# Optimization experiments

Measured on AMD Instinct MI355X. Metric: run time of the kernel, lower is better.

The kernel has to match this reference:

```python
import jax, jax.numpy as jnp
import numpy as np

N = 8192
IN_DIM = 256
OUT_DIM = 128
ALPHA = 0.2  # LeakyReLU negative slope
MASK_VAL = -9e15


def setup_inputs() -> dict:
    key = jax.random.key(0)
    k1, k2, k3, k4 = jax.random.split(key, 4)
    adjacency = jax.random.randint(k1, (N, N), 0, 2, dtype=jnp.int32)
    X = jax.random.normal(k2, (N, IN_DIM), dtype=jnp.float32)
    # kaiming-normal-ish scale
    W = jax.random.normal(k3, (IN_DIM, OUT_DIM), dtype=jnp.float32) * np.sqrt(2.0 / IN_DIM)
    a = jax.random.normal(k4, (2 * OUT_DIM, 1), dtype=jnp.float32) * np.sqrt(2.0 / (2 * OUT_DIM))
    return {"adjacency": adjacency, "X": X, "W": W, "a": a}


def reference(adjacency, X, W, a):
    Wh = X @ W  # [N, D]
    # e[i,j] = lrelu([Wh_i ; Wh_j] @ a) = lrelu(Wh@a1 + (Wh@a2)^T)
    a1 = a[:OUT_DIM, 0]   # [D]
    a2 = a[OUT_DIM:, 0]   # [D]
    e = (Wh @ a1)[:, None] + (Wh @ a2)[None, :]  # [N, N]
    e = jax.nn.leaky_relu(e, negative_slope=ALPHA)
    scores = jnp.where(adjacency > 0, e, jnp.asarray(MASK_VAL, e.dtype))
    attention = jax.nn.softmax(scores, axis=1)  # dropout p=0 -> identity
    h_prime = attention @ Wh  # [N, D]
    return jax.nn.elu(h_prime)
```

## Files before the change

kernel.cpp:

```cpp
#include <hip/hip_runtime.h>
#include <hip/hip_bf16.h>

#define NN 8192
#define KDIM 256
#define DDIM 128

typedef __attribute__((ext_vector_type(8))) short short8;
typedef __attribute__((ext_vector_type(4))) float floatx4;
typedef __attribute__((ext_vector_type(4))) int intx4;

__device__ __forceinline__ unsigned short f2bf(float x) {
    unsigned int u = __float_as_uint(x);
    return (unsigned short)((u + 0x8000u) >> 16);
}
__device__ __forceinline__ float bf2f(unsigned short b) {
    return __uint_as_float(((unsigned int)b) << 16);
}

__global__ void k_trip(float* out, float v) {
    if (threadIdx.x == 0 && blockIdx.x == 0) out[0] = v;
}

__global__ void k_detect(const unsigned short* __restrict__ X16, int* __restrict__ flag) {
    __shared__ int cnt;
    if (threadIdx.x == 0) cnt = 0;
    __syncthreads();
    unsigned short s = X16[2 * threadIdx.x];
    int e = (s >> 7) & 0xFF;
    if (e == 0 || (e >= 100 && e <= 145)) atomicAdd(&cnt, 1);
    __syncthreads();
    if (threadIdx.x == 0) *flag = (cnt >= 200) ? 1 : 0;
}

__global__ void k0_swizzleW(const unsigned short* __restrict__ W16,
                            const float* __restrict__ W32,
                            const int* __restrict__ flag,
                            unsigned short* __restrict__ WB) {
    int isb = *flag;
    int gid = blockIdx.x * blockDim.x + threadIdx.x;
    int kt   = gid >> 9;
    int nt   = (gid >> 6) & 7;
    int lane = gid & 63;
    int quad = lane >> 4, c = lane & 15;
    short8 pack;
    if (isb) {
#pragma unroll
        for (int t = 0; t < 8; ++t)
            pack[t] = (short)W16[(kt * 32 + quad * 8 + t) * DDIM + nt * 16 + c];
    } else {
#pragma unroll
        for (int t = 0; t < 8; ++t)
            pack[t] = (short)f2bf(W32[(kt * 32 + quad * 8 + t) * DDIM + nt * 16 + c]);
    }
    *(short8*)(WB + ((size_t)(kt * 8 + nt) * 64 + lane) * 8) = pack;
}

__global__ __launch_bounds__(256) void k1_wh(
        const unsigned short* __restrict__ X16,
        const float* __restrict__ X32,
        const unsigned short* __restrict__ WB,
        const unsigned short* __restrict__ a16,
        const float* __restrict__ a32,
        const int* __restrict__ flag,
        unsigned short* __restrict__ WhB,
        float* __restrict__ f, float* __restrict__ g) {
    __shared__ unsigned short tile[64 * 128];
    int isb = *flag;
    int tid = threadIdx.x;
    int wave = tid >> 6, lane = tid & 63;
    int quad = lane >> 4, c = lane & 15;
    int rowbase = blockIdx.x * 64 + wave * 16;

    floatx4 acc[8];
#pragma unroll
    for (int nt = 0; nt < 8; ++nt) acc[nt] = (floatx4)(0.0f);

    const short8* WB8 = (const short8*)WB;
#pragma unroll
    for (int ks = 0; ks < 8; ++ks) {
        short8 afrag;
        if (isb) {
            afrag = *(const short8*)(X16 + (size_t)(rowbase + c) * KDIM + ks * 32 + quad * 8);
        } else {
            const float* xp = X32 + (size_t)(rowbase + c) * KDIM + ks * 32 + quad * 8;
            floatx4 x0 = *(const floatx4*)xp;
            floatx4 x1 = *(const floatx4*)(xp + 4);
#pragma unroll
            for (int t = 0; t < 4; ++t) { afrag[t] = (short)f2bf(x0[t]); afrag[4 + t] = (short)f2bf(x1[t]); }
        }
#pragma unroll
        for (int nt = 0; nt < 8; ++nt) {
            short8 b = WB8[(ks * 8 + nt) * 64 + lane];
            acc[nt] = __builtin_amdgcn_mfma_f32_16x16x32_bf16(afrag, b, acc[nt], 0, 0, 0);
        }
    }

    float fp[4] = {0.f, 0.f, 0.f, 0.f}, gp[4] = {0.f, 0.f, 0.f, 0.f};
#pragma unroll
    for (int nt = 0; nt < 8; ++nt) {
        float a1 = isb ? bf2f(a16[nt * 16 + c]) : a32[nt * 16 + c];
        float a2 = isb ? bf2f(a16[DDIM + nt * 16 + c]) : a32[DDIM + nt * 16 + c];
#pragma unroll
        for (int r = 0; r < 4; ++r) {
            fp[r] += acc[nt][r] * a1;
            gp[r] += acc[nt][r] * a2;
        }
    }
#pragma unroll
    for (int m = 1; m < 16; m <<= 1) {
#pragma unroll
        for (int r = 0; r < 4; ++r) {
            fp[r] += __shfl_xor(fp[r], m);
            gp[r] += __shfl_xor(gp[r], m);
        }
    }
    if (c == 0) {
#pragma unroll
        for (int r = 0; r < 4; ++r) {
            f[rowbase + quad * 4 + r] = fp[r];
            g[rowbase + quad * 4 + r] = gp[r];
        }
    }

#pragma unroll
    for (int nt = 0; nt < 8; ++nt)
#pragma unroll
        for (int r = 0; r < 4; ++r)
            tile[(wave * 16 + quad * 4 + r) * 128 + nt * 16 + c] = f2bf(acc[nt][r]);
    __syncthreads();

    int kt2 = wave >> 1;
#pragma unroll
    for (int ntj = 0; ntj < 4; ++ntj) {
        int nt = (wave & 1) * 4 + ntj;
        short8 pack;
#pragma unroll
        for (int t = 0; t < 8; ++t)
            pack[t] = (short)tile[(kt2 * 32 + quad * 8 + t) * 128 + nt * 16 + c];
        *(short8*)(WhB + ((size_t)((blockIdx.x * 2 + kt2) * 8 + nt) * 64 + lane) * 8) = pack;
    }
}

__global__ __launch_bounds__(512) void k2_attn(
        const int* __restrict__ adj,
        const unsigned short* __restrict__ WhB,
        const float* __restrict__ f, const float* __restrict__ g,
        float* __restrict__ out) {
    __shared__ float smem[16384];
    int tid = threadIdx.x;
    int wave = tid >> 6, lane = tid & 63;
    int quad = lane >> 4, c = lane & 15;
    int rowbase = blockIdx.x * 32;

    for (int i = tid; i < NN / 4; i += 512)
        ((floatx4*)smem)[i] = ((const floatx4*)g)[i];
    __syncthreads();

    float f0 = f[rowbase + c];
    float f1 = f[rowbase + 16 + c];

    floatx4 acc0[8], acc1[8];
#pragma unroll
    for (int nt = 0; nt < 8; ++nt) { acc0[nt] = (floatx4)(0.0f); acc1[nt] = (floatx4)(0.0f); }
    float l0 = 0.0f, l1 = 0.0f;

    const intx4* arow0 = (const intx4*)(adj + (long)(rowbase + c) * NN);
    const intx4* arow1 = (const intx4*)(adj + (long)(rowbase + 16 + c) * NN);
    const short8* WhB8 = (const short8*)WhB;

    int j40 = wave * 8 + quad * 2;
    intx4 c00 = arow0[j40], c01 = arow0[j40 + 1];
    intx4 c10 = arow1[j40], c11 = arow1[j40 + 1];
    floatx4 g0 = *(const floatx4*)&smem[wave * 32 + quad * 8];
    floatx4 g1 = *(const floatx4*)&smem[wave * 32 + quad * 8 + 4];

    for (int t = 0; t < 32; ++t) {
        int tn = (t + 1) & 31;
        int j4n = (tn * 8 + wave) * 8 + quad * 2;
        intx4 n00 = arow0[j4n], n01 = arow0[j4n + 1];
        intx4 n10 = arow1[j4n], n11 = arow1[j4n + 1];
        int jbn = (tn * 8 + wave) * 32 + quad * 8;
        floatx4 gn0 = *(const floatx4*)&smem[jbn];
        floatx4 gn1 = *(const floatx4*)&smem[jbn + 4];

        int J32 = t * 8 + wave;
        short8 bfr[8];
#pragma unroll
        for (int nt = 0; nt < 8; ++nt)
            bfr[nt] = WhB8[((size_t)J32 * 8 + nt) * 64 + lane];

        short8 afr0, afr1;
#pragma unroll
        for (int u = 0; u < 4; ++u) {
            float x, E;
            unsigned short eb;
            x = f0 + g0[u]; x = fminf(fmaxf(x, 0.2f * x), 80.0f);
            E = (c00[u] > 0) ? __expf(x) : 0.0f; eb = f2bf(E); l0 += bf2f(eb); afr0[u] = (short)eb;
            x = f0 + g1[u]; x = fminf(fmaxf(x, 0.2f * x), 80.0f);
            E = (c01[u] > 0) ? __expf(x) : 0.0f; eb = f2bf(E); l0 += bf2f(eb); afr0[4 + u] = (short)eb;
            x = f1 + g0[u]; x = fminf(fmaxf(x, 0.2f * x), 80.0f);
            E = (c10[u] > 0) ? __expf(x) : 0.0f; eb = f2bf(E); l1 += bf2f(eb); afr1[u] = (short)eb;
            x = f1 + g1[u]; x = fminf(fmaxf(x, 0.2f * x), 80.0f);
            E = (c11[u] > 0) ? __expf(x) : 0.0f; eb = f2bf(E); l1 += bf2f(eb); afr1[4 + u] = (short)eb;
        }

#pragma unroll
        for (int nt = 0; nt < 8; ++nt) {
            acc0[nt] = __builtin_amdgcn_mfma_f32_16x16x32_bf16(afr0, bfr[nt], acc0[nt], 0, 0, 0);
            acc1[nt] = __builtin_amdgcn_mfma_f32_16x16x32_bf16(afr1, bfr[nt], acc1[nt], 0, 0, 0);
        }

        c00 = n00; c01 = n01; c10 = n10; c11 = n11;
        g0 = gn0; g1 = gn1;
    }

    __syncthreads();
    smem[wave * 128 + lane] = l0;
    smem[wave * 128 + 64 + lane] = l1;
    __syncthreads();
    if (tid < 32) {
        int mt = tid >> 4, cc = tid & 15;
        float s = 0.0f;
#pragma unroll
        for (int w = 0; w < 8; ++w)
#pragma unroll
            for (int q = 0; q < 4; ++q)
                s += smem[w * 128 + mt * 64 + q * 16 + cc];
        smem[1024 + tid] = s;
    }
    __syncthreads();
    float linv0[4], linv1[4];
    if (wave == 0) {
#pragma unroll
        for (int r = 0; r < 4; ++r) {
            float l0v = smem[1024 + quad * 4 + r];
            float l1v = smem[1024 + 16 + quad * 4 + r];
            linv0[r] = (l0v > 0.0f) ? 1.0f / l0v : 0.0f;
            linv1[r] = (l1v > 0.0f) ? 1.0f / l1v : 0.0f;
        }
    }
    __syncthreads();

    for (int half = 4; half >= 1; half >>= 1) {
        if (wave >= half && wave < 2 * half) {
            floatx4* buf = (floatx4*)&smem[(wave - half) * 4096 + lane * 64];
#pragma unroll
            for (int nt = 0; nt < 8; ++nt) { buf[nt] = acc0[nt]; buf[8 + nt] = acc1[nt]; }
        }
        __syncthreads();
        if (wave < half) {
            floatx4* buf = (floatx4*)&smem[wave * 4096 + lane * 64];
#pragma unroll
            for (int nt = 0; nt < 8; ++nt) { acc0[nt] += buf[nt]; acc1[nt] += buf[8 + nt]; }
        }
        __syncthreads();
    }

    if (wave == 0) {
#pragma unroll
        for (int nt = 0; nt < 8; ++nt) {
#pragma unroll
            for (int r = 0; r < 4; ++r) {
                float h = acc0[nt][r] * linv0[r];
                h = (h > 0.0f) ? h : expm1f(h);
                out[(size_t)(rowbase + quad * 4 + r) * DDIM + nt * 16 + c] = h;
                float h2 = acc1[nt][r] * linv1[r];
                h2 = (h2 > 0.0f) ? h2 : expm1f(h2);
                out[(size_t)(rowbase + 16 + quad * 4 + r) * DDIM + nt * 16 + c] = h2;
            }
        }
    }
}

extern "C" void kernel_launch(void* const* d_in, const int* in_sizes, int n_in,
                              void* d_out, int out_size, void* d_ws, size_t ws_size,
                              hipStream_t stream) {
    float* out = (float*)d_out;

    const void *p_adj = nullptr, *p_X = nullptr, *p_W = nullptr, *p_a = nullptr;
    for (int i = 0; i < n_in; ++i) {
        switch (in_sizes[i]) {
            case NN * NN:     p_adj = d_in[i]; break;
            case NN * KDIM:   p_X   = d_in[i]; break;
            case KDIM * DDIM: p_W   = d_in[i]; break;
            case 2 * DDIM:    p_a   = d_in[i]; break;
            default: break;
        }
    }
    if (!p_adj || !p_X || !p_W || !p_a) {
        k_trip<<<dim3(1), dim3(64), 0, stream>>>(out, 99999.0f);
        return;
    }

    size_t off_WB  = 0;
    size_t off_WhB = off_WB + 65536;
    size_t off_f   = off_WhB + (size_t)NN * DDIM * 2;
    size_t off_g   = off_f + NN * 4;
    size_t off_fl  = off_g + NN * 4;
    size_t needed  = off_fl + 64;
    if (ws_size < needed) {
        k_trip<<<dim3(1), dim3(64), 0, stream>>>(out, 12345.0f);
        return;
    }
    char* ws = (char*)d_ws;
    unsigned short* WB   = (unsigned short*)(ws + off_WB);
    unsigned short* WhB  = (unsigned short*)(ws + off_WhB);
    float*          f    = (float*)(ws + off_f);
    float*          g    = (float*)(ws + off_g);
    int*            flag = (int*)(ws + off_fl);

    const int* adj = (const int*)p_adj;
    const unsigned short* X16 = (const unsigned short*)p_X;
    const float*          X32 = (const float*)p_X;
    const unsigned short* W16 = (const unsigned short*)p_W;
    const float*          W32 = (const float*)p_W;
    const unsigned short* a16 = (const unsigned short*)p_a;
    const float*          a32 = (const float*)p_a;

    k_detect<<<dim3(1), dim3(256), 0, stream>>>(X16, flag);
    k0_swizzleW<<<dim3(16), dim3(256), 0, stream>>>(W16, W32, flag, WB);
    k1_wh<<<dim3(128), dim3(256), 0, stream>>>(X16, X32, WB, a16, a32, flag, WhB, f, g);
    k2_attn<<<dim3(256), dim3(512), 0, stream>>>(adj, WhB, f, g, out);
}
```

Before: 415.9 us.

## Shrink attention blocks to 16 rows and drop bf16 input detection

The attention kernel now gives each block 16 rows, 256 threads and half the shared memory, launching 512 blocks with a launch-bounds occupancy hint of 3. Adjacency loads are prefetched two iterations ahead, g is read from shared memory each iteration, and the cross-wave reduction is simplified. The bf16/fp32 detection kernel and its branches are removed, and the exp clamp and bf16 roundtrip in the row sum are dropped. Each block reloads g and WhB for half as many rows, which lowers data reuse.

```diff
diff --git a/kernel.cpp b/kernel.cpp
--- a/kernel.cpp
+++ b/kernel.cpp
@@ -13,59 +13,29 @@
     unsigned int u = __float_as_uint(x);
     return (unsigned short)((u + 0x8000u) >> 16);
 }
-__device__ __forceinline__ float bf2f(unsigned short b) {
-    return __uint_as_float(((unsigned int)b) << 16);
-}
 
 __global__ void k_trip(float* out, float v) {
     if (threadIdx.x == 0 && blockIdx.x == 0) out[0] = v;
 }
 
-__global__ void k_detect(const unsigned short* __restrict__ X16, int* __restrict__ flag) {
-    __shared__ int cnt;
-    if (threadIdx.x == 0) cnt = 0;
-    __syncthreads();
-    unsigned short s = X16[2 * threadIdx.x];
-    int e = (s >> 7) & 0xFF;
-    if (e == 0 || (e >= 100 && e <= 145)) atomicAdd(&cnt, 1);
-    __syncthreads();
-    if (threadIdx.x == 0) *flag = (cnt >= 200) ? 1 : 0;
-}
-
-__global__ void k0_swizzleW(const unsigned short* __restrict__ W16,
-                            const float* __restrict__ W32,
-                            const int* __restrict__ flag,
-                            unsigned short* __restrict__ WB) {
-    int isb = *flag;
+__global__ void kA_swizzleW(const float* __restrict__ W, unsigned short* __restrict__ WB) {
     int gid = blockIdx.x * blockDim.x + threadIdx.x;
-    int kt   = gid >> 9;
-    int nt   = (gid >> 6) & 7;
-    int lane = gid & 63;
+    int kt = gid >> 9, nt = (gid >> 6) & 7, lane = gid & 63;
     int quad = lane >> 4, c = lane & 15;
     short8 pack;
-    if (isb) {
-#pragma unroll
-        for (int t = 0; t < 8; ++t)
-            pack[t] = (short)W16[(kt * 32 + quad * 8 + t) * DDIM + nt * 16 + c];
-    } else {
-#pragma unroll
-        for (int t = 0; t < 8; ++t)
-            pack[t] = (short)f2bf(W32[(kt * 32 + quad * 8 + t) * DDIM + nt * 16 + c]);
-    }
+#pragma unroll
+    for (int t = 0; t < 8; ++t)
+        pack[t] = (short)f2bf(W[(kt * 32 + quad * 8 + t) * DDIM + nt * 16 + c]);
     *(short8*)(WB + ((size_t)(kt * 8 + nt) * 64 + lane) * 8) = pack;
 }
 
-__global__ __launch_bounds__(256) void k1_wh(
-        const unsigned short* __restrict__ X16,
-        const float* __restrict__ X32,
+__global__ __launch_bounds__(256) void kB_wh(
+        const float* __restrict__ X,
         const unsigned short* __restrict__ WB,
-        const unsigned short* __restrict__ a16,
-        const float* __restrict__ a32,
-        const int* __restrict__ flag,
+        const float* __restrict__ a,
         unsigned short* __restrict__ WhB,
         float* __restrict__ f, float* __restrict__ g) {
     __shared__ unsigned short tile[64 * 128];
-    int isb = *flag;
     int tid = threadIdx.x;
     int wave = tid >> 6, lane = tid & 63;
     int quad = lane >> 4, c = lane & 15;
@@ -78,16 +48,12 @@
     const short8* WB8 = (const short8*)WB;
 #pragma unroll
     for (int ks = 0; ks < 8; ++ks) {
+        const float* xp = X + (size_t)(rowbase + c) * KDIM + ks * 32 + quad * 8;
+        floatx4 x0 = *(const floatx4*)xp;
+        floatx4 x1 = *(const floatx4*)(xp + 4);
         short8 afrag;
-        if (isb) {
-            afrag = *(const short8*)(X16 + (size_t)(rowbase + c) * KDIM + ks * 32 + quad * 8);
-        } else {
-            const float* xp = X32 + (size_t)(rowbase + c) * KDIM + ks * 32 + quad * 8;
-            floatx4 x0 = *(const floatx4*)xp;
-            floatx4 x1 = *(const floatx4*)(xp + 4);
-#pragma unroll
-            for (int t = 0; t < 4; ++t) { afrag[t] = (short)f2bf(x0[t]); afrag[4 + t] = (short)f2bf(x1[t]); }
-        }
+#pragma unroll
+        for (int t = 0; t < 4; ++t) { afrag[t] = (short)f2bf(x0[t]); afrag[4 + t] = (short)f2bf(x1[t]); }
 #pragma unroll
         for (int nt = 0; nt < 8; ++nt) {
             short8 b = WB8[(ks * 8 + nt) * 64 + lane];
@@ -98,8 +64,8 @@
     float fp[4] = {0.f, 0.f, 0.f, 0.f}, gp[4] = {0.f, 0.f, 0.f, 0.f};
 #pragma unroll
     for (int nt = 0; nt < 8; ++nt) {
-        float a1 = isb ? bf2f(a16[nt * 16 + c]) : a32[nt * 16 + c];
-        float a2 = isb ? bf2f(a16[DDIM + nt * 16 + c]) : a32[DDIM + nt * 16 + c];
+        float a1 = a[nt * 16 + c];
+        float a2 = a[DDIM + nt * 16 + c];
 #pragma unroll
         for (int r = 0; r < 4; ++r) {
             fp[r] += acc[nt][r] * a1;
@@ -141,134 +107,113 @@
     }
 }
 
-__global__ __launch_bounds__(512) void k2_attn(
+__global__ __launch_bounds__(256, 3) void kC_attn(
         const int* __restrict__ adj,
         const unsigned short* __restrict__ WhB,
         const float* __restrict__ f, const float* __restrict__ g,
         float* __restrict__ out) {
-    __shared__ float smem[16384];
+    __shared__ float smem[8192];
     int tid = threadIdx.x;
     int wave = tid >> 6, lane = tid & 63;
     int quad = lane >> 4, c = lane & 15;
-    int rowbase = blockIdx.x * 32;
-
-    for (int i = tid; i < NN / 4; i += 512)
+    int rowbase = blockIdx.x * 16;
+
+    for (int i = tid; i < NN / 4; i += 256)
         ((floatx4*)smem)[i] = ((const floatx4*)g)[i];
     __syncthreads();
 
     float f0 = f[rowbase + c];
-    float f1 = f[rowbase + 16 + c];
-
-    floatx4 acc0[8], acc1[8];
-#pragma unroll
-    for (int nt = 0; nt < 8; ++nt) { acc0[nt] = (floatx4)(0.0f); acc1[nt] = (floatx4)(0.0f); }
-    float l0 = 0.0f, l1 = 0.0f;
-
-    const intx4* arow0 = (const intx4*)(adj + (long)(rowbase + c) * NN);
-    const intx4* arow1 = (const intx4*)(adj + (long)(rowbase + 16 + c) * NN);
+
+    floatx4 acc[8];
+#pragma unroll
+    for (int nt = 0; nt < 8; ++nt) acc[nt] = (floatx4)(0.0f);
+    float l0 = 0.0f;
+
+    const intx4* arow = (const intx4*)(adj + (size_t)(rowbase + c) * NN);
     const short8* WhB8 = (const short8*)WhB;
 
-    int j40 = wave * 8 + quad * 2;
-    intx4 c00 = arow0[j40], c01 = arow0[j40 + 1];
-    intx4 c10 = arow1[j40], c11 = arow1[j40 + 1];
-    floatx4 g0 = *(const floatx4*)&smem[wave * 32 + quad * 8];
-    floatx4 g1 = *(const floatx4*)&smem[wave * 32 + quad * 8 + 4];
-
-    for (int t = 0; t < 32; ++t) {
-        int tn = (t + 1) & 31;
-        int j4n = (tn * 8 + wave) * 8 + quad * 2;
-        intx4 n00 = arow0[j4n], n01 = arow0[j4n + 1];
-        intx4 n10 = arow1[j4n], n11 = arow1[j4n + 1];
-        int jbn = (tn * 8 + wave) * 32 + quad * 8;
-        floatx4 gn0 = *(const floatx4*)&smem[jbn];
-        floatx4 gn1 = *(const floatx4*)&smem[jbn + 4];
-
-        int J32 = t * 8 + wave;
+    intx4 A0a = arow[(0 * 4 + wave) * 8 + quad * 2], A0b = arow[(0 * 4 + wave) * 8 + quad * 2 + 1];
+    intx4 A1a = arow[(1 * 4 + wave) * 8 + quad * 2], A1b = arow[(1 * 4 + wave) * 8 + quad * 2 + 1];
+
+    for (int it = 0; it < 64; ++it) {
+        int j4n = (((it + 2) & 63) * 4 + wave) * 8 + quad * 2;
+        intx4 A2a = arow[j4n], A2b = arow[j4n + 1];
+
+        int J32 = it * 4 + wave;
         short8 bfr[8];
 #pragma unroll
         for (int nt = 0; nt < 8; ++nt)
             bfr[nt] = WhB8[((size_t)J32 * 8 + nt) * 64 + lane];
 
-        short8 afr0, afr1;
+        int gb = J32 * 32 + quad * 8;
+        floatx4 g0 = *(const floatx4*)&smem[gb];
+        floatx4 g1 = *(const floatx4*)&smem[gb + 4];
+
+        short8 afr;
 #pragma unroll
         for (int u = 0; u < 4; ++u) {
             float x, E;
-            unsigned short eb;
-            x = f0 + g0[u]; x = fminf(fmaxf(x, 0.2f * x), 80.0f);
-            E = (c00[u] > 0) ? __expf(x) : 0.0f; eb = f2bf(E); l0 += bf2f(eb); afr0[u] = (short)eb;
-            x = f0 + g1[u]; x = fminf(fmaxf(x, 0.2f * x), 80.0f);
-            E = (c01[u] > 0) ? __expf(x) : 0.0f; eb = f2bf(E); l0 += bf2f(eb); afr0[4 + u] = (short)eb;
-            x = f1 + g0[u]; x = fminf(fmaxf(x, 0.2f * x), 80.0f);
-            E = (c10[u] > 0) ? __expf(x) : 0.0f; eb = f2bf(E); l1 += bf2f(eb); afr1[u] = (short)eb;
-            x = f1 + g1[u]; x = fminf(fmaxf(x, 0.2f * x), 80.0f);
-            E = (c11[u] > 0) ? __expf(x) : 0.0f; eb = f2bf(E); l1 += bf2f(eb); afr1[4 + u] = (short)eb;
-        }
-
-#pragma unroll
-        for (int nt = 0; nt < 8; ++nt) {
-            acc0[nt] = __builtin_amdgcn_mfma_f32_16x16x32_bf16(afr0, bfr[nt], acc0[nt], 0, 0, 0);
-            acc1[nt] = __builtin_amdgcn_mfma_f32_16x16x32_bf16(afr1, bfr[nt], acc1[nt], 0, 0, 0);
-        }
-
-        c00 = n00; c01 = n01; c10 = n10; c11 = n11;
-        g0 = gn0; g1 = gn1;
-    }
-
-    __syncthreads();
-    smem[wave * 128 + lane] = l0;
-    smem[wave * 128 + 64 + lane] = l1;
-    __syncthreads();
-    if (tid < 32) {
-        int mt = tid >> 4, cc = tid & 15;
+            x = f0 + g0[u]; x = fmaxf(x, 0.2f * x);
+            E = (A0a[u] > 0) ? __expf(x) : 0.0f; l0 += E; afr[u] = (short)f2bf(E);
+            x = f0 + g1[u]; x = fmaxf(x, 0.2f * x);
+            E = (A0b[u] > 0) ? __expf(x) : 0.0f; l0 += E; afr[4 + u] = (short)f2bf(E);
+        }
+
+#pragma unroll
+        for (int nt = 0; nt < 8; ++nt)
+            acc[nt] = __builtin_amdgcn_mfma_f32_16x16x32_bf16(afr, bfr[nt], acc[nt], 0, 0, 0);
+
+        A0a = A1a; A0b = A1b; A1a = A2a; A1b = A2b;
+    }
+
+    __syncthreads();
+    smem[7000 + wave * 64 + lane] = l0;
+    __syncthreads();
+    if (tid < 16) {
         float s = 0.0f;
 #pragma unroll
-        for (int w = 0; w < 8; ++w)
+        for (int w = 0; w < 4; ++w)
 #pragma unroll
             for (int q = 0; q < 4; ++q)
-                s += smem[w * 128 + mt * 64 + q * 16 + cc];
-        smem[1024 + tid] = s;
-    }
-    __syncthreads();
-    float linv0[4], linv1[4];
+                s += smem[7000 + w * 64 + q * 16 + tid];
+        smem[7256 + tid] = (s > 0.0f) ? 1.0f / s : 0.0f;
+    }
+    __syncthreads();
+
+    if (wave >= 2) {
+        float* b = &smem[(wave - 2) * 2304 + lane * 36];
+#pragma unroll
+        for (int nt = 0; nt < 8; ++nt) *(floatx4*)&b[nt * 4] = acc[nt];
+    }
+    __syncthreads();
+    if (wave < 2) {
+        float* b = &smem[wave * 2304 + lane * 36];
+#pragma unroll
+        for (int nt = 0; nt < 8; ++nt) acc[nt] += *(const floatx4*)&b[nt * 4];
+    }
+    __syncthreads();
+    if (wave == 1) {
+        float* b = &smem[lane * 36];
+#pragma unroll
+        for (int nt = 0; nt < 8; ++nt) *(floatx4*)&b[nt * 4] = acc[nt];
+    }
+    __syncthreads();
+
     if (wave == 0) {
-#pragma unroll
-        for (int r = 0; r < 4; ++r) {
-            float l0v = smem[1024 + quad * 4 + r];
-            float l1v = smem[1024 + 16 + quad * 4 + r];
-            linv0[r] = (l0v > 0.0f) ? 1.0f / l0v : 0.0f;
-            linv1[r] = (l1v > 0.0f) ? 1.0f / l1v : 0.0f;
-        }
-    }
-    __syncthreads();
-
-    for (int half = 4; half >= 1; half >>= 1) {
-        if (wave >= half && wave < 2 * half) {
-            floatx4* buf = (floatx4*)&smem[(wave - half) * 4096 + lane * 64];
-#pragma unroll
-            for (int nt = 0; nt < 8; ++nt) { buf[nt] = acc0[nt]; buf[8 + nt] = acc1[nt]; }
-        }
-        __syncthreads();
-        if (wave < half) {
-            floatx4* buf = (floatx4*)&smem[wave * 4096 + lane * 64];
-#pragma unroll
-            for (int nt = 0; nt < 8; ++nt) { acc0[nt] += buf[nt]; acc1[nt] += buf[8 + nt]; }
-        }
-        __syncthreads();
-    }
-
-    if (wave == 0) {
-#pragma unroll
-        for (int nt = 0; nt < 8; ++nt) {
+        float* b = &smem[lane * 36];
+#pragma unroll
+        for (int nt = 0; nt < 8; ++nt) acc[nt] += *(const floatx4*)&b[nt * 4];
+        float linv[4];
+#pragma unroll
+        for (int r = 0; r < 4; ++r) linv[r] = smem[7256 + quad * 4 + r];
+#pragma unroll
+        for (int nt = 0; nt < 8; ++nt)
 #pragma unroll
             for (int r = 0; r < 4; ++r) {
-                float h = acc0[nt][r] * linv0[r];
+                float h = acc[nt][r] * linv[r];
                 h = (h > 0.0f) ? h : expm1f(h);
                 out[(size_t)(rowbase + quad * 4 + r) * DDIM + nt * 16 + c] = h;
-                float h2 = acc1[nt][r] * linv1[r];
-                h2 = (h2 > 0.0f) ? h2 : expm1f(h2);
-                out[(size_t)(rowbase + 16 + quad * 4 + r) * DDIM + nt * 16 + c] = h2;
             }
-        }
     }
 }
 
@@ -296,29 +241,23 @@
     size_t off_WhB = off_WB + 65536;
     size_t off_f   = off_WhB + (size_t)NN * DDIM * 2;
     size_t off_g   = off_f + NN * 4;
-    size_t off_fl  = off_g + NN * 4;
-    size_t needed  = off_fl + 64;
+    size_t needed  = off_g + NN * 4;
     if (ws_size < needed) {
         k_trip<<<dim3(1), dim3(64), 0, stream>>>(out, 12345.0f);
         return;
     }
     char* ws = (char*)d_ws;
-    unsigned short* WB   = (unsigned short*)(ws + off_WB);
-    unsigned short* WhB  = (unsigned short*)(ws + off_WhB);
-    float*          f    = (float*)(ws + off_f);
-    float*          g    = (float*)(ws + off_g);
-    int*            flag = (int*)(ws + off_fl);
-
-    const int* adj = (const int*)p_adj;
-    const unsigned short* X16 = (const unsigned short*)p_X;
-    const float*          X32 = (const float*)p_X;
-    const unsigned short* W16 = (const unsigned short*)p_W;
-    const float*          W32 = (const float*)p_W;
-    const unsigned short* a16 = (const unsigned short*)p_a;
-    const float*          a32 = (const float*)p_a;
-
-    k_detect<<<dim3(1), dim3(256), 0, stream>>>(X16, flag);
-    k0_swizzleW<<<dim3(16), dim3(256), 0, stream>>>(W16, W32, flag, WB);
-    k1_wh<<<dim3(128), dim3(256), 0, stream>>>(X16, X32, WB, a16, a32, flag, WhB, f, g);
-    k2_attn<<<dim3(256), dim3(512), 0, stream>>>(adj, WhB, f, g, out);
-}
+    unsigned short* WB  = (unsigned short*)(ws + off_WB);
+    unsigned short* WhB = (unsigned short*)(ws + off_WhB);
+    float*          f   = (float*)(ws + off_f);
+    float*          g   = (float*)(ws + off_g);
+
+    const int*   adj = (const int*)p_adj;
+    const float* X   = (const float*)p_X;
+    const float* W   = (const float*)p_W;
+    const float* a   = (const float*)p_a;
+
+    kA_swizzleW<<<dim3(16), dim3(256), 0, stream>>>(W, WB);
+    kB_wh<<<dim3(128), dim3(256), 0, stream>>>(X, WB, a, WhB, f, g);
+    kC_attn<<<dim3(512), dim3(256), 0, stream>>>(adj, WhB, f, g, out);
+}
```

New measurement: 413.4 us (median of 2 runs). Within noise of the previous version (-0.6%).
